# Kernel tuning notes

Hardware: AMD Instinct MI355X
Metric: run time of the kernel (lower is better)

## Reference

```python
import jax, jax.numpy as jnp
from jax import lax
import numpy as np

B, T, H, IN = 256, 1024, 256, 1

def setup_inputs() -> dict:
    key = jax.random.key(0)
    ks = jax.random.split(key, 9)
    s = 1.0 / np.sqrt(H)  # PyTorch default uniform(-1/sqrt(H), 1/sqrt(H)); use scaled normal
    return {
        "x": jax.random.normal(ks[0], (B, T, IN), jnp.float32),
        "W_ih0": jax.random.normal(ks[1], (4 * H, IN), jnp.float32) * s,
        "W_hh0": jax.random.normal(ks[2], (4 * H, H), jnp.float32) * s,
        "b_ih0": jax.random.normal(ks[3], (4 * H,), jnp.float32) * s,
        "b_hh0": jax.random.normal(ks[4], (4 * H,), jnp.float32) * s,
        "W_ih1": jax.random.normal(ks[5], (4 * H, H), jnp.float32) * s,
        "W_hh1": jax.random.normal(ks[6], (4 * H, H), jnp.float32) * s,
        "b_ih1": jax.random.normal(ks[7], (4 * H,), jnp.float32) * s,
        "b_hh1": jax.random.normal(ks[8], (4 * H,), jnp.float32) * s,
    }

def _lstm_layer(x, W_ih, W_hh, b_ih, b_hh):
    # x: [B, T, D_in] -> (y [B, T, H], h_T [B, H], c_T [B, H]); gates ordered i,f,g,o (PyTorch)
    b, t = x.shape[0], x.shape[1]
    h = W_hh.shape[1]
    # precompute input projection for all timesteps: [T, B, 4H]
    xp = jnp.swapaxes(jnp.einsum('btd,gd->btg', x, W_ih) + b_ih + b_hh, 0, 1)

    def step(carry, xt):
        hprev, cprev = carry
        gates = xt + hprev @ W_hh.T  # [B, 4H]
        i, f, g, o = jnp.split(gates, 4, axis=-1)
        i = jax.nn.sigmoid(i)
        f = jax.nn.sigmoid(f)
        g = jnp.tanh(g)
        o = jax.nn.sigmoid(o)
        c = f * cprev + i * g
        hnew = o * jnp.tanh(c)
        return (hnew, c), hnew

    h0 = jnp.zeros((b, h), x.dtype)
    (hT, cT), ys = lax.scan(step, (h0, h0), xp)
    return jnp.swapaxes(ys, 0, 1), hT, cT

def reference(x, W_ih0, W_hh0, b_ih0, b_hh0, W_ih1, W_hh1, b_ih1, b_hh1):
    y0, h0, c0 = _lstm_layer(x, W_ih0, W_hh0, b_ih0, b_hh0)
    # inter-layer dropout(0.1) is train-only; inference = identity
    _, h1, c1 = _lstm_layer(y0, W_ih1, W_hh1, b_ih1, b_hh1)
    h_n = jnp.stack([h0, h1], axis=0)  # [num_layers, B, H]
    c_n = jnp.stack([c0, c1], axis=0)
    return h_n, c_n
```

## Files before the change

### kernel.cpp

```cpp
#include <hip/hip_runtime.h>


#define TSTEPS 1024u

typedef __attribute__((ext_vector_type(8))) short bf16x8;
typedef __attribute__((ext_vector_type(4))) float f32x4;

__device__ __forceinline__ unsigned short f2bf(float f) {
  unsigned u = __float_as_uint(f);
  u += 0x7FFFu + ((u >> 16) & 1u);
  return (unsigned short)(u >> 16);
}
__device__ __forceinline__ float sigm(float x) { return 1.0f / (1.0f + __expf(-x)); }
__device__ __forceinline__ float tanh_f(float x) {
  float xc = fminf(fmaxf(x, -15.0f), 15.0f);
  float e = __expf(2.0f * xc);
  return (e - 1.0f) / (e + 1.0f);
}

__global__ __launch_bounds__(256, 1) void lstm2_v5(
    const float* __restrict__ x,
    const float* __restrict__ Wih0,
    const float* __restrict__ Whh0,
    const float* __restrict__ bih0, const float* __restrict__ bhh0,
    const float* __restrict__ Wih1,
    const float* __restrict__ Whh1,
    const float* __restrict__ bih1, const float* __restrict__ bhh1,
    float* __restrict__ out,
    unsigned long long* __restrict__ fastb,
    unsigned long long* __restrict__ slowb,
    unsigned* __restrict__ ctrl)
{
  const int bid  = blockIdx.x;
  const int c    = bid & 15;
  const int iw   = bid >> 4;
  const int tid  = threadIdx.x;
  const int lane = tid & 63;
  const int wv   = tid >> 6;
  const int hi   = lane >> 4;
  const int lm   = lane & 15;

  const unsigned long long TB = 0x4000400040004000ULL;

  unsigned myxcc;
  asm volatile("s_getreg_b32 %0, hwreg(HW_REG_XCC_ID)" : "=s"(myxcc));
  myxcc &= 0xFu;
  if (tid == 0)
    __hip_atomic_store(&ctrl[bid], 0x5A5A0000u | myxcc,
                       __ATOMIC_RELAXED, __HIP_MEMORY_SCOPE_AGENT);

  bf16x8 w0[8], wi1[8], wh1[8];
  {
    const int wrow = (lm & 3) * 256 + (iw << 4) + (wv << 2) + (lm >> 2);
    const int kb   = hi << 3;
#pragma unroll
    for (int kk = 0; kk < 8; ++kk) {
      const int k0 = kk * 32 + kb;
      const float* p0 = Whh0 + (size_t)wrow * 256 + k0;
      const float* p1 = Wih1 + (size_t)wrow * 256 + k0;
      const float* p2 = Whh1 + (size_t)wrow * 256 + k0;
      bf16x8 a, b, cc;
#pragma unroll
      for (int e = 0; e < 8; ++e) {
        a[e]  = (short)f2bf(p0[e]);
        b[e]  = (short)f2bf(p1[e]);
        cc[e] = (short)f2bf(p2[e]);
      }
      w0[kk] = a; wi1[kk] = b; wh1[kk] = cc;
    }
  }

  const int rowE = lm;
  const int jg   = (iw << 4) + (wv << 2) + hi;
  float wx[4], bs0[4], bs1[4];
#pragma unroll
  for (int r = 0; r < 4; ++r) {
    const int col = (r << 8) + jg;
    wx[r]  = Wih0[col];
    bs0[r] = bih0[col] + bhh0[col];
    bs1[r] = bih1[col] + bhh1[col];
  }

  unsigned ofs0[4], lofs0[4];
#pragma unroll
  for (int i = 0; i < 4; ++i) {
    const int n   = tid + 256 * i;
    const int row = (n >> 6) & 15;
    const int q   = n & 63;
    ofs0[i]  = (unsigned)(((c * 2 + 0) * 16 + row) * 64 + q);
    lofs0[i] = (unsigned)(row * 264 + q * 4);
  }

  __shared__ unsigned s_uni;
  if (tid == 0) {
    if (iw == 0) {
      unsigned x0 = 0, uni = 1u;
      for (int k = 0; k < 16 && uni; ++k) {
        unsigned v; int g2 = 0;
        for (;;) {
          v = __hip_atomic_load(&ctrl[c + 16 * k], __ATOMIC_RELAXED, __HIP_MEMORY_SCOPE_AGENT);
          if ((v & 0xFFFF0000u) == 0x5A5A0000u) break;
          if (++g2 > (1 << 15)) { uni = 0u; break; }
        }
        if (uni) {
          const unsigned xc = v & 0xFFFFu;
          if (k == 0) x0 = xc; else if (xc != x0) uni = 0u;
        }
      }
      __hip_atomic_store(&ctrl[256 + c], 0x5A5A0000u | uni,
                         __ATOMIC_RELAXED, __HIP_MEMORY_SCOPE_AGENT);
    }
    unsigned uni = 0u; int g2 = 0;
    for (;;) {
      unsigned v = __hip_atomic_load(&ctrl[256 + c], __ATOMIC_RELAXED, __HIP_MEMORY_SCOPE_AGENT);
      if ((v & 0xFFFF0000u) == 0x5A5A0000u) { uni = v & 1u; break; }
      if (++g2 > (1 << 15)) break;
    }
    s_uni = uni;
  }
  __syncthreads();
  const bool uniform = (s_uni != 0u);
  unsigned long long* pollb = uniform ? fastb : slowb;

  __shared__ __align__(16) unsigned short A[2 * 16 * 264];

  const float* xrow = x + (size_t)((c << 4) + rowE) * TSTEPS;

  float c0 = 0.f, h0f = 0.f, c1 = 0.f, h1f = 0.f;
  bool dead = false;

  for (unsigned s = 0; s <= TSTEPS; ++s) {
    const float xv = (s < TSTEPS) ? xrow[s] : 0.f;

    const unsigned t4 = s & 15u;
    const unsigned long long em =
        ((unsigned long long)(t4 & 1u)        << 14) |
        ((unsigned long long)((t4 >> 1) & 1u) << 30) |
        ((unsigned long long)((t4 >> 2) & 1u) << 46) |
        ((unsigned long long)((t4 >> 3) & 1u) << 62);
    const unsigned tau = s + 1u;
    const unsigned long long emn =
        ((unsigned long long)(tau & 1u)        << 14) |
        ((unsigned long long)((tau >> 1) & 1u) << 30) |
        ((unsigned long long)((tau >> 2) & 1u) << 46) |
        ((unsigned long long)((tau >> 3) & 1u) << 62);
    unsigned long long* fb = fastb + (size_t)(tau & 1u) * 32768u;
    unsigned long long* sb = slowb + (size_t)(tau & 1u) * 32768u;
    const unsigned long long* pb = pollb + (size_t)(s & 1u) * 32768u;

    if (s == 0) {
      for (int z = tid; z < 2112; z += 256) ((unsigned*)A)[z] = 0u;
    } else {
      unsigned long long vv[4] = {0, 0, 0, 0};
      int guard = 0;
      while (!dead) {
#pragma unroll
        for (int i = 0; i < 4; ++i)
          vv[i] = __hip_atomic_load(pb + ofs0[i], __ATOMIC_RELAXED, __HIP_MEMORY_SCOPE_AGENT);
        const bool ok = ((vv[0] & TB) == em) & ((vv[1] & TB) == em) &
                        ((vv[2] & TB) == em) & ((vv[3] & TB) == em);
        if (__all(ok)) break;
        if (++guard > (1 << 14)) dead = true;
      }
#pragma unroll
      for (int i = 0; i < 4; ++i)
        *(unsigned long long*)&A[lofs0[i]] = vv[i] & ~TB;
    }
    __syncthreads();

    bf16x8 af0[8];
    f32x4 acc0 = {0.f, 0.f, 0.f, 0.f};
    {
      const unsigned short* a0p = &A[lm * 264 + (hi << 3)];
#pragma unroll
      for (int kk = 0; kk < 8; ++kk) {
        af0[kk] = *(const bf16x8*)(a0p + kk * 32);
        acc0 = __builtin_amdgcn_mfma_f32_16x16x32_bf16(w0[kk], af0[kk], acc0, 0, 0, 0);
      }
    }

    if (s < TSTEPS) {
      const float pi = acc0[0] + xv * wx[0] + bs0[0];
      const float pf = acc0[1] + xv * wx[1] + bs0[1];
      const float pg = acc0[2] + xv * wx[2] + bs0[2];
      const float po = acc0[3] + xv * wx[3] + bs0[3];
      const float ig = sigm(pi), fg = sigm(pf), gv = tanh_f(pg), og = sigm(po);
      c0  = fg * c0 + ig * gv;
      h0f = og * tanh_f(c0);

      const int v  = (int)(unsigned)f2bf(h0f);
      const int p16 = __shfl_xor(v, 16);
      const unsigned part = (unsigned)(unsigned short)v | ((unsigned)(unsigned short)p16 << 16);
      const unsigned p32  = (unsigned)__shfl_xor((int)part, 32);
      unsigned long long v64 = (unsigned long long)part | ((unsigned long long)p32 << 32);
      v64 = (v64 & ~TB) | emn;
      const unsigned i0 = ((c * 2 + 0) * 16 + (unsigned)rowE) * 64 + (unsigned)((iw << 2) + wv);
      if (hi == 0) {
        __hip_atomic_store(fb + i0, v64, __ATOMIC_RELAXED, __HIP_MEMORY_SCOPE_WORKGROUP);
        if (!uniform)
          __hip_atomic_store(sb + i0, v64, __ATOMIC_RELAXED, __HIP_MEMORY_SCOPE_AGENT);
      }
    }

    if (s >= 1u) {
      unsigned long long vv[4] = {0, 0, 0, 0};
      int guard = 0;
      while (!dead) {
#pragma unroll
        for (int i = 0; i < 4; ++i)
          vv[i] = __hip_atomic_load(pb + (ofs0[i] + 1024u),
                                    __ATOMIC_RELAXED, __HIP_MEMORY_SCOPE_AGENT);
        const bool ok = ((vv[0] & TB) == em) & ((vv[1] & TB) == em) &
                        ((vv[2] & TB) == em) & ((vv[3] & TB) == em);
        if (__all(ok)) break;
        if (++guard > (1 << 14)) dead = true;
      }
#pragma unroll
      for (int i = 0; i < 4; ++i)
        *(unsigned long long*)&A[lofs0[i] + 4224u] = vv[i] & ~TB;
    }
    __syncthreads();

    f32x4 acc1a = {0.f, 0.f, 0.f, 0.f};
    f32x4 acc1b = {0.f, 0.f, 0.f, 0.f};
    {
      const unsigned short* a1p = &A[4224 + lm * 264 + (hi << 3)];
#pragma unroll
      for (int kk = 0; kk < 8; ++kk) {
        acc1a = __builtin_amdgcn_mfma_f32_16x16x32_bf16(wi1[kk], af0[kk], acc1a, 0, 0, 0);
        const bf16x8 a1f = *(const bf16x8*)(a1p + kk * 32);
        acc1b = __builtin_amdgcn_mfma_f32_16x16x32_bf16(wh1[kk], a1f, acc1b, 0, 0, 0);
      }
    }

    if (s >= 1u) {
      const float pi = acc1a[0] + acc1b[0] + bs1[0];
      const float pf = acc1a[1] + acc1b[1] + bs1[1];
      const float pg = acc1a[2] + acc1b[2] + bs1[2];
      const float po = acc1a[3] + acc1b[3] + bs1[3];
      const float ig = sigm(pi), fg = sigm(pf), gv = tanh_f(pg), og = sigm(po);
      c1  = fg * c1 + ig * gv;
      h1f = og * tanh_f(c1);
    }
    if (s < TSTEPS) {
      const int v  = (int)(unsigned)f2bf(h1f);
      const int p16 = __shfl_xor(v, 16);
      const unsigned part = (unsigned)(unsigned short)v | ((unsigned)(unsigned short)p16 << 16);
      const unsigned p32  = (unsigned)__shfl_xor((int)part, 32);
      unsigned long long v64 = (unsigned long long)part | ((unsigned long long)p32 << 32);
      v64 = (v64 & ~TB) | emn;
      const unsigned i1 = ((c * 2 + 1) * 16 + (unsigned)rowE) * 64 + (unsigned)((iw << 2) + wv);
      if (hi == 0) {
        __hip_atomic_store(fb + i1, v64, __ATOMIC_RELAXED, __HIP_MEMORY_SCOPE_WORKGROUP);
        if (!uniform)
          __hip_atomic_store(sb + i1, v64, __ATOMIC_RELAXED, __HIP_MEMORY_SCOPE_AGENT);
      }
    }
  }

  {
    const int b  = (c << 4) + rowE;
    const size_t o = (size_t)b * 256 + jg;
    out[o]                  = h0f;
    out[65536 + o]          = h1f;
    out[131072 + o]         = c0;
    out[131072 + 65536 + o] = c1;
  }
}

extern "C" void kernel_launch(void* const* d_in, const int* in_sizes, int n_in,
                              void* d_out, int out_size, void* d_ws, size_t ws_size,
                              hipStream_t stream) {
  const float* x    = (const float*)d_in[0];
  const float* Wih0 = (const float*)d_in[1];
  const float* Whh0 = (const float*)d_in[2];
  const float* bih0 = (const float*)d_in[3];
  const float* bhh0 = (const float*)d_in[4];
  const float* Wih1 = (const float*)d_in[5];
  const float* Whh1 = (const float*)d_in[6];
  const float* bih1 = (const float*)d_in[7];
  const float* bhh1 = (const float*)d_in[8];

  unsigned long long* fastb = (unsigned long long*)d_ws;
  unsigned long long* slowb;
  unsigned* ctrl;
  if (ws_size >= (1u << 20) + 2048u) {
    slowb = fastb + 65536;
    ctrl  = (unsigned*)(fastb + 131072);
  } else {
    slowb = fastb;
    ctrl  = (unsigned*)((char*)d_ws + (512u << 10));
  }

  lstm2_v5<<<256, 256, 0, stream>>>(x, Wih0, Whh0, bih0, bhh0,
                                    Wih1, Whh1, bih1, bhh1,
                                    (float*)d_out, fastb, slowb, ctrl);
}
```

Measured before the change: 2.077 ms.

## Merge layer-0 and layer-1 polls into one barrier with double-buffered LDS

Each step now polls the layer-0 and layer-1 exchange buffers together in a single spin loop and a single __syncthreads, instead of two separate poll-and-barrier phases. The LDS staging area is double-buffered by step parity so the one barrier per step stays safe. MFMA chains are split into two independent accumulators each to shorten dependency chains, and x is loaded four steps at a time as a float4. The aim is to remove one global synchronisation round trip per timestep on the critical path, at the cost of more LDS, more registers, and making layer-0 compute wait on the layer-1 data.

```diff
diff --git a/kernel.cpp b/kernel.cpp
--- a/kernel.cpp
+++ b/kernel.cpp
@@ -18,7 +18,7 @@
   return (e - 1.0f) / (e + 1.0f);
 }
 
-__global__ __launch_bounds__(256, 1) void lstm2_v5(
+__global__ __launch_bounds__(256, 1) void lstm2_v6(
     const float* __restrict__ x,
     const float* __restrict__ Wih0,
     const float* __restrict__ Whh0,
@@ -81,14 +81,15 @@
     bs1[r] = bih1[col] + bhh1[col];
   }
 
-  unsigned ofs0[4], lofs0[4];
-#pragma unroll
-  for (int i = 0; i < 4; ++i) {
+  unsigned ofs_[8], lofs_[8];
+#pragma unroll
+  for (int i = 0; i < 8; ++i) {
     const int n   = tid + 256 * i;
+    const int L   = n >> 10;
     const int row = (n >> 6) & 15;
     const int q   = n & 63;
-    ofs0[i]  = (unsigned)(((c * 2 + 0) * 16 + row) * 64 + q);
-    lofs0[i] = (unsigned)(row * 264 + q * 4);
+    ofs_[i]  = (unsigned)(((c * 2 + L) * 16 + row) * 64 + q);
+    lofs_[i] = (unsigned)(L * 4224 + row * 264 + q * 4);
   }
 
   __shared__ unsigned s_uni;
@@ -122,15 +123,17 @@
   const bool uniform = (s_uni != 0u);
   unsigned long long* pollb = uniform ? fastb : slowb;
 
-  __shared__ __align__(16) unsigned short A[2 * 16 * 264];
+  __shared__ __align__(16) unsigned short A[2 * 2 * 16 * 264];
 
   const float* xrow = x + (size_t)((c << 4) + rowE) * TSTEPS;
+  float4 xq = {0.f, 0.f, 0.f, 0.f};
 
   float c0 = 0.f, h0f = 0.f, c1 = 0.f, h1f = 0.f;
   bool dead = false;
 
   for (unsigned s = 0; s <= TSTEPS; ++s) {
-    const float xv = (s < TSTEPS) ? xrow[s] : 0.f;
+    if ((s & 3u) == 0u && s < TSTEPS) xq = *(const float4*)(xrow + s);
+    const float xv = (s & 2u) ? ((s & 1u) ? xq.w : xq.z) : ((s & 1u) ? xq.y : xq.x);
 
     const unsigned t4 = s & 15u;
     const unsigned long long em =
@@ -147,48 +150,69 @@
     unsigned long long* fb = fastb + (size_t)(tau & 1u) * 32768u;
     unsigned long long* sb = slowb + (size_t)(tau & 1u) * 32768u;
     const unsigned long long* pb = pollb + (size_t)(s & 1u) * 32768u;
+    unsigned short* Ap = A + (s & 1u) * 8448u;
 
     if (s == 0) {
-      for (int z = tid; z < 2112; z += 256) ((unsigned*)A)[z] = 0u;
+      for (int z = tid; z < 8448; z += 256) ((unsigned*)A)[z] = 0u;
     } else {
-      unsigned long long vv[4] = {0, 0, 0, 0};
+      unsigned long long vv[8];
       int guard = 0;
       while (!dead) {
 #pragma unroll
-        for (int i = 0; i < 4; ++i)
-          vv[i] = __hip_atomic_load(pb + ofs0[i], __ATOMIC_RELAXED, __HIP_MEMORY_SCOPE_AGENT);
-        const bool ok = ((vv[0] & TB) == em) & ((vv[1] & TB) == em) &
-                        ((vv[2] & TB) == em) & ((vv[3] & TB) == em);
+        for (int i = 0; i < 8; ++i)
+          vv[i] = __hip_atomic_load(pb + ofs_[i], __ATOMIC_RELAXED, __HIP_MEMORY_SCOPE_AGENT);
+        bool ok = true;
+#pragma unroll
+        for (int i = 0; i < 8; ++i) ok &= ((vv[i] & TB) == em);
         if (__all(ok)) break;
         if (++guard > (1 << 14)) dead = true;
       }
 #pragma unroll
-      for (int i = 0; i < 4; ++i)
-        *(unsigned long long*)&A[lofs0[i]] = vv[i] & ~TB;
+      for (int i = 0; i < 8; ++i)
+        *(unsigned long long*)&Ap[lofs_[i]] = vv[i] & ~TB;
     }
     __syncthreads();
 
     bf16x8 af0[8];
-    f32x4 acc0 = {0.f, 0.f, 0.f, 0.f};
-    {
-      const unsigned short* a0p = &A[lm * 264 + (hi << 3)];
-#pragma unroll
-      for (int kk = 0; kk < 8; ++kk) {
-        af0[kk] = *(const bf16x8*)(a0p + kk * 32);
-        acc0 = __builtin_amdgcn_mfma_f32_16x16x32_bf16(w0[kk], af0[kk], acc0, 0, 0, 0);
-      }
+    f32x4 acc0a = {0.f, 0.f, 0.f, 0.f}, acc0b = {0.f, 0.f, 0.f, 0.f};
+    const unsigned short* a0p = Ap + lm * 264 + (hi << 3);
+    const unsigned short* a1p = a0p + 4224;
+#pragma unroll
+    for (int kk = 0; kk < 4; ++kk) {
+      af0[kk] = *(const bf16x8*)(a0p + kk * 32);
+      acc0a = __builtin_amdgcn_mfma_f32_16x16x32_bf16(w0[kk], af0[kk], acc0a, 0, 0, 0);
+    }
+#pragma unroll
+    for (int kk = 4; kk < 8; ++kk) {
+      af0[kk] = *(const bf16x8*)(a0p + kk * 32);
+      acc0b = __builtin_amdgcn_mfma_f32_16x16x32_bf16(w0[kk], af0[kk], acc0b, 0, 0, 0);
+    }
+
+    f32x4 a1a0 = {0.f, 0.f, 0.f, 0.f}, a1a1 = {0.f, 0.f, 0.f, 0.f};
+    f32x4 a1b0 = {0.f, 0.f, 0.f, 0.f}, a1b1 = {0.f, 0.f, 0.f, 0.f};
+#pragma unroll
+    for (int kk = 0; kk < 4; ++kk) {
+      a1a0 = __builtin_amdgcn_mfma_f32_16x16x32_bf16(wi1[kk], af0[kk], a1a0, 0, 0, 0);
+      const bf16x8 a1f = *(const bf16x8*)(a1p + kk * 32);
+      a1b0 = __builtin_amdgcn_mfma_f32_16x16x32_bf16(wh1[kk], a1f, a1b0, 0, 0, 0);
+    }
+#pragma unroll
+    for (int kk = 4; kk < 8; ++kk) {
+      a1a1 = __builtin_amdgcn_mfma_f32_16x16x32_bf16(wi1[kk], af0[kk], a1a1, 0, 0, 0);
+      const bf16x8 a1f = *(const bf16x8*)(a1p + kk * 32);
+      a1b1 = __builtin_amdgcn_mfma_f32_16x16x32_bf16(wh1[kk], a1f, a1b1, 0, 0, 0);
     }
 
     if (s < TSTEPS) {
-      const float pi = acc0[0] + xv * wx[0] + bs0[0];
-      const float pf = acc0[1] + xv * wx[1] + bs0[1];
-      const float pg = acc0[2] + xv * wx[2] + bs0[2];
-      const float po = acc0[3] + xv * wx[3] + bs0[3];
+      const float pi = (acc0a[0] + acc0b[0]) + xv * wx[0] + bs0[0];
+      const float pf = (acc0a[1] + acc0b[1]) + xv * wx[1] + bs0[1];
+      const float pg = (acc0a[2] + acc0b[2]) + xv * wx[2] + bs0[2];
+      const float po = (acc0a[3] + acc0b[3]) + xv * wx[3] + bs0[3];
       const float ig = sigm(pi), fg = sigm(pf), gv = tanh_f(pg), og = sigm(po);
       c0  = fg * c0 + ig * gv;
       h0f = og * tanh_f(c0);
 
-      const int v  = (int)(unsigned)f2bf(h0f);
+      const int v   = (int)(unsigned)f2bf(h0f);
       const int p16 = __shfl_xor(v, 16);
       const unsigned part = (unsigned)(unsigned short)v | ((unsigned)(unsigned short)p16 << 16);
       const unsigned p32  = (unsigned)__shfl_xor((int)part, 32);
@@ -203,47 +227,16 @@
     }
 
     if (s >= 1u) {
-      unsigned long long vv[4] = {0, 0, 0, 0};
-      int guard = 0;
-      while (!dead) {
-#pragma unroll
-        for (int i = 0; i < 4; ++i)
-          vv[i] = __hip_atomic_load(pb + (ofs0[i] + 1024u),
-                                    __ATOMIC_RELAXED, __HIP_MEMORY_SCOPE_AGENT);
-        const bool ok = ((vv[0] & TB) == em) & ((vv[1] & TB) == em) &
-                        ((vv[2] & TB) == em) & ((vv[3] & TB) == em);
-        if (__all(ok)) break;
-        if (++guard > (1 << 14)) dead = true;
-      }
-#pragma unroll
-      for (int i = 0; i < 4; ++i)
-        *(unsigned long long*)&A[lofs0[i] + 4224u] = vv[i] & ~TB;
-    }
-    __syncthreads();
-
-    f32x4 acc1a = {0.f, 0.f, 0.f, 0.f};
-    f32x4 acc1b = {0.f, 0.f, 0.f, 0.f};
-    {
-      const unsigned short* a1p = &A[4224 + lm * 264 + (hi << 3)];
-#pragma unroll
-      for (int kk = 0; kk < 8; ++kk) {
-        acc1a = __builtin_amdgcn_mfma_f32_16x16x32_bf16(wi1[kk], af0[kk], acc1a, 0, 0, 0);
-        const bf16x8 a1f = *(const bf16x8*)(a1p + kk * 32);
-        acc1b = __builtin_amdgcn_mfma_f32_16x16x32_bf16(wh1[kk], a1f, acc1b, 0, 0, 0);
-      }
-    }
-
-    if (s >= 1u) {
-      const float pi = acc1a[0] + acc1b[0] + bs1[0];
-      const float pf = acc1a[1] + acc1b[1] + bs1[1];
-      const float pg = acc1a[2] + acc1b[2] + bs1[2];
-      const float po = acc1a[3] + acc1b[3] + bs1[3];
+      const float pi = (a1a0[0] + a1a1[0]) + (a1b0[0] + a1b1[0]) + bs1[0];
+      const float pf = (a1a0[1] + a1a1[1]) + (a1b0[1] + a1b1[1]) + bs1[1];
+      const float pg = (a1a0[2] + a1a1[2]) + (a1b0[2] + a1b1[2]) + bs1[2];
+      const float po = (a1a0[3] + a1a1[3]) + (a1b0[3] + a1b1[3]) + bs1[3];
       const float ig = sigm(pi), fg = sigm(pf), gv = tanh_f(pg), og = sigm(po);
       c1  = fg * c1 + ig * gv;
       h1f = og * tanh_f(c1);
     }
     if (s < TSTEPS) {
-      const int v  = (int)(unsigned)f2bf(h1f);
+      const int v   = (int)(unsigned)f2bf(h1f);
       const int p16 = __shfl_xor(v, 16);
       const unsigned part = (unsigned)(unsigned short)v | ((unsigned)(unsigned short)p16 << 16);
       const unsigned p32  = (unsigned)__shfl_xor((int)part, 32);
@@ -292,7 +285,7 @@
     ctrl  = (unsigned*)((char*)d_ws + (512u << 10));
   }
 
-  lstm2_v5<<<256, 256, 0, stream>>>(x, Wih0, Whh0, bih0, bhh0,
+  lstm2_v6<<<256, 256, 0, stream>>>(x, Wih0, Whh0, bih0, bhh0,
                                     Wih1, Whh1, bih1, bhh1,
                                     (float*)d_out, fastb, slowb, ctrl);
 }
```

Result: faster. 1.812 ms (-12.7%).
